# Performance work log

Hardware: AMD Instinct MI355X
Metric: run time of the kernel (lower is better)

The kernel has to match this reference:

```python
import math
import jax, jax.numpy as jnp
import numpy as np

B, N, D, H, L = 8, 128, 256, 8, 4
NOBJ, NREL = 150, 51
FF = 4 * D
Hd = D // H

def setup_inputs() -> dict:
    key = jax.random.key(0)
    ks = iter(jax.random.split(key, 80))
    def nrm(shape):
        return 0.02 * jax.random.normal(next(ks), shape, dtype=jnp.float32)
    inp = {}
    inp['obj_t'] = jax.random.randint(next(ks), (B, N), 0, NOBJ + 1)
    inp['rel_t'] = jax.random.randint(next(ks), (B, N, N), 0, NREL)
    inp['t'] = jax.random.randint(next(ks), (B,), 0, 1000)
    inp['node_mask'] = jnp.ones((B, N), dtype=bool)
    inp['edge_mask'] = jnp.ones((B, N, N), dtype=bool)
    # embeddings
    inp['obj_emb_table'] = nrm((NOBJ + 1, D))
    inp['rel_emb_table'] = nrm((NREL, D))
    # time mlp
    inp['time_w1'] = nrm((D, D)); inp['time_b1'] = jnp.zeros((D,), jnp.float32)
    inp['time_w2'] = nrm((D, D)); inp['time_b2'] = jnp.zeros((D,), jnp.float32)
    # per-layer stacked params [L, ...]
    inp['ln1_g'] = jnp.ones((L, D), jnp.float32); inp['ln1_b'] = jnp.zeros((L, D), jnp.float32)
    inp['q_w'] = nrm((L, D, D)); inp['q_b'] = jnp.zeros((L, D), jnp.float32)
    inp['k_w'] = nrm((L, D, D)); inp['k_b'] = jnp.zeros((L, D), jnp.float32)
    inp['v_w'] = nrm((L, D, D)); inp['v_b'] = jnp.zeros((L, D), jnp.float32)
    inp['o_w'] = nrm((L, D, D)); inp['o_b'] = jnp.zeros((L, D), jnp.float32)
    inp['eb_w'] = nrm((L, D, H)); inp['eb_b'] = jnp.zeros((L, H), jnp.float32)
    inp['ln2_g'] = jnp.ones((L, D), jnp.float32); inp['ln2_b'] = jnp.zeros((L, D), jnp.float32)
    inp['ff_w1'] = nrm((L, D, FF)); inp['ff_b1'] = jnp.zeros((L, FF), jnp.float32)
    inp['ff_w2'] = nrm((L, FF, D)); inp['ff_b2'] = jnp.zeros((L, D), jnp.float32)
    # heads
    inp['obj_head_w'] = nrm((D, NOBJ)); inp['obj_head_b'] = jnp.zeros((NOBJ,), jnp.float32)
    inp['subj_w'] = nrm((D, D)); inp['subj_b'] = jnp.zeros((D,), jnp.float32)
    inp['objp_w'] = nrm((D, D)); inp['objp_b'] = jnp.zeros((D,), jnp.float32)
    inp['eh_w1'] = nrm((4 * D, D)); inp['eh_b1'] = jnp.zeros((D,), jnp.float32)
    inp['eh_w2'] = nrm((D, 1)); inp['eh_b2'] = jnp.zeros((1,), jnp.float32)
    inp['rh_w1'] = nrm((4 * D, D)); inp['rh_b1'] = jnp.zeros((D,), jnp.float32)
    inp['rh_w2'] = nrm((D, NREL - 1)); inp['rh_b2'] = jnp.zeros((NREL - 1,), jnp.float32)
    return inp

def _ln(x, g, b, eps=1e-5):
    m = x.mean(-1, keepdims=True)
    v = ((x - m) ** 2).mean(-1, keepdims=True)
    return (x - m) / jnp.sqrt(v + eps) * g + b

def _timestep_emb(t, dim):
    half = dim // 2
    freqs = jnp.exp(-math.log(10000.0) * jnp.arange(half, dtype=jnp.float32) / half)
    args = t.astype(jnp.float32)[:, None] * freqs[None, :]
    return jnp.concatenate([jnp.cos(args), jnp.sin(args)], axis=-1)

def _gelu(x):
    return jax.nn.gelu(x, approximate=False)

def _forward(obj_t, rel_t, t, node_mask, edge_mask, p):
    nm = node_mask[..., None].astype(jnp.float32)  # [B,N,1]
    h = p['obj_emb_table'][obj_t]                  # [B,N,D]
    temb = _timestep_emb(t, D)
    temb = jax.nn.silu(temb @ p['time_w1'] + p['time_b1']) @ p['time_w2'] + p['time_b2']
    h = (h + temb[:, None, :]) * nm
    rel_emb = p['rel_emb_table'][rel_t]            # [B,N,N,D]
    scale = Hd ** -0.5
    for l in range(L):
        x = _ln(h, p['ln1_g'][l], p['ln1_b'][l])
        q = (x @ p['q_w'][l] + p['q_b'][l]).reshape(B, N, H, Hd)
        k = (x @ p['k_w'][l] + p['k_b'][l]).reshape(B, N, H, Hd)
        v = (x @ p['v_w'][l] + p['v_b'][l]).reshape(B, N, H, Hd)
        logits = jnp.einsum('bihd,bjhd->bhij', q, k) * scale
        bias = jnp.einsum('bijd,dh->bhij', rel_emb, p['eb_w'][l]) + p['eb_b'][l][None, :, None, None]
        logits = logits + bias
        logits = jnp.where(edge_mask[:, None, :, :], logits, -jnp.inf)
        logits = jnp.where(node_mask[:, None, None, :], logits, -jnp.inf)
        attn = jax.nn.softmax(logits, axis=-1)
        attn = jnp.nan_to_num(attn, nan=0.0, posinf=0.0, neginf=0.0)
        out = jnp.einsum('bhij,bjhd->bihd', attn, v).reshape(B, N, D)
        h = h + out @ p['o_w'][l] + p['o_b'][l]
        x2 = _ln(h, p['ln2_g'][l], p['ln2_b'][l])
        h = h + _gelu(x2 @ p['ff_w1'][l] + p['ff_b1'][l]) @ p['ff_w2'][l] + p['ff_b2'][l]
        h = h * nm
    obj_logits = h @ p['obj_head_w'] + p['obj_head_b']      # [B,N,NOBJ]
    subj_h = h @ p['subj_w'] + p['subj_b']
    obj_h = h @ p['objp_w'] + p['objp_b']
    hi = jnp.broadcast_to(subj_h[:, :, None, :], (B, N, N, D))
    hj = jnp.broadcast_to(obj_h[:, None, :, :], (B, N, N, D))
    pair_feat = jnp.concatenate([hi, hj, hi - hj, hi * hj], axis=-1)  # [B,N,N,4D]
    edge_logits = (_gelu(pair_feat @ p['eh_w1'] + p['eh_b1']) @ p['eh_w2'] + p['eh_b2'])[..., 0]
    rel_logits_pos = _gelu(pair_feat @ p['rh_w1'] + p['rh_b1']) @ p['rh_w2'] + p['rh_b2']
    return obj_logits, edge_logits, rel_logits_pos

PARAM_NAMES = ['obj_emb_table','rel_emb_table','time_w1','time_b1','time_w2','time_b2','ln1_g','ln1_b','q_w','q_b','k_w','k_b','v_w','v_b','o_w','o_b','eb_w','eb_b','ln2_g','ln2_b','ff_w1','ff_b1','ff_w2','ff_b2','obj_head_w','obj_head_b','subj_w','subj_b','objp_w','objp_b','eh_w1','eh_b1','eh_w2','eh_b2','rh_w1','rh_b1','rh_w2','rh_b2']

def reference(obj_t, rel_t, t, node_mask, edge_mask, obj_emb_table, rel_emb_table, time_w1, time_b1, time_w2, time_b2, ln1_g, ln1_b, q_w, q_b, k_w, k_b, v_w, v_b, o_w, o_b, eb_w, eb_b, ln2_g, ln2_b, ff_w1, ff_b1, ff_w2, ff_b2, obj_head_w, obj_head_b, subj_w, subj_b, objp_w, objp_b, eh_w1, eh_b1, eh_w2, eh_b2, rh_w1, rh_b1, rh_w2, rh_b2):
    loc = locals()
    p = {n: loc[n] for n in PARAM_NAMES}
    return _forward(obj_t, rel_t, t, node_mask, edge_mask, p)
```

## Files before the change

### kernel.cpp

```cpp
#include <hip/hip_runtime.h>
#include <hip/hip_bf16.h>
#include <math.h>

#define BB 8
#define NN 128
#define DD 256
#define HH 8
#define LL 4
#define FFD 1024
#define HD 32
#define NOBJ_ 150
#define NREL_ 51

typedef __attribute__((ext_vector_type(4))) float f32x4;
typedef __attribute__((ext_vector_type(8))) short s16x8;

__device__ __forceinline__ float erf_f(float x){
    float ax = fabsf(x);
    float t = __builtin_amdgcn_rcpf(1.f + 0.3275911f*ax);
    float y = t*(0.254829592f + t*(-0.284496736f + t*(1.421413741f +
              t*(-1.453152027f + t*1.061405429f))));
    float r = 1.f - y*__expf(-ax*ax);
    return copysignf(r, x);
}
__device__ __forceinline__ float gelu_f(float x){
    return 0.5f * x * (1.0f + erf_f(x * 0.70710678118654752f));
}
__device__ __forceinline__ ushort f2bf(float f){
    uint u = __float_as_uint(f);
    u += 0x7fff + ((u >> 16) & 1);
    return (ushort)(u >> 16);
}
__device__ __forceinline__ float bf2f(uint u){
    return __uint_as_float((u & 0xffffu) << 16);
}

__global__ __launch_bounds__(256) void k_init_h(const int* __restrict__ obj_t,
        const float* __restrict__ emb, const float* __restrict__ temb,
        float* __restrict__ h){
    int idx = blockIdx.x*256 + threadIdx.x;
    int d = idx & 255, n = (idx >> 8) & 127, b = idx >> 15;
    int o = obj_t[b*NN + n];
    h[idx] = emb[o*DD + d] + temb[b*DD + d];
}

__global__ __launch_bounds__(256) void k_lngemm(
        const float* __restrict__ A, const float* __restrict__ gw,
        const float* __restrict__ bw, const ushort* __restrict__ WT,
        const float* __restrict__ bias, ushort* __restrict__ Cb,
        int Nc, int act){
    __shared__ __align__(16) ushort As[8192];
    __shared__ __align__(16) ushort Ws[16384];
    int tid = threadIdx.x;
    int m0 = blockIdx.x*32, n0 = blockIdx.y*64;
    int r = tid >> 3, p = tid & 7;
    const float* ap = A + (size_t)(m0 + r)*256 + p*32;
    float x[32];
    float s1 = 0.f, s2 = 0.f;
    #pragma unroll
    for (int e4 = 0; e4 < 8; e4++){
        float4 v = *(const float4*)(ap + e4*4);
        x[e4*4+0]=v.x; x[e4*4+1]=v.y; x[e4*4+2]=v.z; x[e4*4+3]=v.w;
        s1 += v.x+v.y+v.z+v.w;
        s2 += v.x*v.x+v.y*v.y+v.z*v.z+v.w*v.w;
    }
    #pragma unroll
    for (int d = 1; d < 8; d <<= 1){
        s1 += __shfl_xor(s1, d, 64);
        s2 += __shfl_xor(s2, d, 64);
    }
    float mean = s1*(1.f/256.f);
    float var = s2*(1.f/256.f) - mean*mean;
    float rstd = rsqrtf(var + 1e-5f);
    #pragma unroll
    for (int j = 0; j < 4; j++){
        int kq = p*4 + j;
        uint o[4];
        #pragma unroll
        for (int pp = 0; pp < 4; pp++){
            int e = j*8 + pp*2;
            int k = p*32 + e;
            float v0 = (x[e]   - mean)*rstd*gw[k]   + bw[k];
            float v1 = (x[e+1] - mean)*rstd*gw[k+1] + bw[k+1];
            o[pp] = (uint)f2bf(v0) | ((uint)f2bf(v1) << 16);
        }
        int phys = r*32 + (kq ^ (r & 7));
        *(uint4*)(As + (size_t)phys*8) = make_uint4(o[0], o[1], o[2], o[3]);
    }
    #pragma unroll
    for (int rr = 0; rr < 8; rr++){
        int gi = tid + rr*256;
        int n = gi >> 5, kq = gi & 31;
        uint4 v = *(const uint4*)(WT + (size_t)(n0+n)*256 + kq*8);
        *(uint4*)(Ws + (size_t)(n*32 + (kq ^ (n&7)))*8) = v;
    }
    __syncthreads();
    int lane = tid & 63, w = tid >> 6, l15 = lane & 15, q = lane >> 4;
    f32x4 acc[2];
    acc[0] = (f32x4){0.f,0.f,0.f,0.f};
    acc[1] = (f32x4){0.f,0.f,0.f,0.f};
    int m = (w&1)*16 + l15;
    #pragma unroll
    for (int k0 = 0; k0 < 8; k0++){
        int kq = k0*4 + q;
        s16x8 af = *(const s16x8*)(As + (size_t)(m*32 + (kq ^ (m&7)))*8);
        #pragma unroll
        for (int t = 0; t < 2; t++){
            int n = ((w>>1)*2 + t)*16 + l15;
            s16x8 bf = *(const s16x8*)(Ws + (size_t)(n*32 + (kq ^ (n&7)))*8);
            acc[t] = __builtin_amdgcn_mfma_f32_16x16x32_bf16(af, bf, acc[t], 0, 0, 0);
        }
    }
    int mb = (w&1)*16;
    #pragma unroll
    for (int t = 0; t < 2; t++){
        int n = n0 + ((w>>1)*2 + t)*16 + l15;
        if (n < Nc){
// ... 252 lines not shown
        const float* __restrict__ objpw,
        const float* __restrict__ q_b, const float* __restrict__ k_b,
        const float* __restrict__ v_b,
        const float* __restrict__ subj_b, const float* __restrict__ objp_b,
        ushort* __restrict__ qkvT, ushort* __restrict__ oT,
        ushort* __restrict__ ff1T, ushort* __restrict__ ff2T,
        ushort* __restrict__ headT, ushort* __restrict__ sowT,
        float* __restrict__ qkvb, float* __restrict__ sob_b){
    int g = blockIdx.x*256 + threadIdx.x;
    if (g < 98304){
        int l = g / 24576, rem = g % 24576;
        int n = rem >> 5, kq = rem & 31;
        const float* src = (n < 256) ? q_w : (n < 512) ? k_w : v_w;
        int nn = n & 255;
        src += (size_t)l*65536;
        #pragma unroll
        for (int u = 0; u < 8; u++)
            qkvT[(size_t)g*8 + u] = f2bf(src[(size_t)(kq*8+u)*256 + nn]);
    } else if ((g -= 98304) < 32768){
        int l = g >> 13, rem = g & 8191;
        int n = rem >> 5, kq = rem & 31;
        const float* src = o_w + (size_t)l*65536;
        #pragma unroll
        for (int u = 0; u < 8; u++)
            oT[(size_t)g*8 + u] = f2bf(src[(size_t)(kq*8+u)*256 + n]);
    } else if ((g -= 32768) < 131072){
        int l = g >> 15, rem = g & 32767;
        int n = rem >> 5, kq = rem & 31;
        const float* src = ff1 + (size_t)l*262144;
        #pragma unroll
        for (int u = 0; u < 8; u++)
            ff1T[(size_t)g*8 + u] = f2bf(src[(size_t)(kq*8+u)*1024 + n]);
    } else if ((g -= 131072) < 131072){
        int l = g >> 15, rem = g & 32767;
        int n = rem >> 7, kq = rem & 127;
        const float* src = ff2 + (size_t)l*262144;
        #pragma unroll
        for (int u = 0; u < 8; u++)
            ff2T[(size_t)g*8 + u] = f2bf(src[(size_t)(kq*8+u)*256 + n]);
    } else if ((g -= 131072) < 6144){
        int n = g >> 5, kq = g & 31;
        #pragma unroll
        for (int u = 0; u < 8; u++)
            headT[(size_t)g*8 + u] = (n < NOBJ_) ? f2bf(headw[(size_t)(kq*8+u)*NOBJ_ + n]) : (ushort)0;
    } else if ((g -= 6144) < 16384){
        int n = g >> 5, kq = g & 31;
        const float* src = (n < 256) ? subjw : objpw;
        int nn = n & 255;
        #pragma unroll
        for (int u = 0; u < 8; u++)
            sowT[(size_t)g*8 + u] = f2bf(src[(size_t)(kq*8+u)*256 + nn]);
    } else if ((g -= 16384) < 384){
        #pragma unroll
        for (int u = 0; u < 8; u++){
            int flat = g*8 + u;
            int l = flat / 768, c = flat % 768;
            qkvb[flat] = (c < 256) ? q_b[l*256 + c] :
                         (c < 512) ? k_b[l*256 + c - 256] : v_b[l*256 + c - 512];
        }
    } else if ((g -= 384) < 64){
        #pragma unroll
        for (int u = 0; u < 8; u++){
            int c = g*8 + u;
            sob_b[c] = (c < 256) ? subj_b[c] : objp_b[c-256];
        }
    }
}

__global__ __launch_bounds__(256) void k_prep_obj(const float* __restrict__ sjhob,
        ushort* __restrict__ objf){
    int t = blockIdx.x*256 + threadIdx.x;
    int ai = t & 1023, kc = (t >> 10) & 3, b = t >> 12;
    int jt = ai >> 7, ks = (ai >> 6) & 1, lane = ai & 63;
    int j = jt*16 + (lane & 15);
    int k0 = kc*64 + ks*32 + (lane >> 4)*8;
    const float* src = sjhob + (size_t)(b*128 + j)*512 + 256 + k0;
    uint o[4];
    #pragma unroll
    for (int p = 0; p < 4; p++)
        o[p] = (uint)f2bf(src[p*2]) | ((uint)f2bf(src[p*2 + 1]) << 16);
    *(uint4*)(objf + (size_t)t*8) = make_uint4(o[0], o[1], o[2], o[3]);
}

__global__ __launch_bounds__(256, 3) void k_pair(
        const float* __restrict__ sjhob, const float* __restrict__ linI,
        const float* __restrict__ linJ, const ushort* __restrict__ objf,
        const ushort* __restrict__ w3fE, const ushort* __restrict__ w3fR,
        const ushort* __restrict__ w2fR, const float* __restrict__ eh_w2,
        const float* __restrict__ eh_b2, const float* __restrict__ rh_b2,
        float* __restrict__ edge_out, float* __restrict__ rel_out){
    __shared__ __align__(16) ushort U[8192];
    __shared__ __align__(16) float Rel[32*52];
    __shared__ __align__(16) float subj_sf[256];
    __shared__ __align__(16) float linEs[256];
    __shared__ __align__(16) float linRs[256];
    __shared__ __align__(16) float w2s[256];
    __shared__ __align__(16) float P[4][32];
    int tid = threadIdx.x;
    int bid = blockIdx.x;
    int jq = bid & 3, i = (bid >> 2) & 127, b = bid >> 9;
    int lane = tid & 63, w = tid >> 6;
    int l15 = lane & 15, q = lane >> 4;
    size_t rw = (size_t)(b*128 + i)*512;
    subj_sf[tid] = sjhob[rw + tid];
    linEs[tid]   = linI[rw + tid];
    linRs[tid]   = linI[rw + 256 + tid];
    w2s[tid]     = eh_w2[tid];
    __syncthreads();

    {
        int ks = (tid >> 6) & 1, qg = (tid >> 4) & 3;
        #pragma unroll
        for (int kc = 0; kc < 4; kc++){
            uint4 po = *(const uint4*)(objf + ((size_t)(b*4 + kc)*1024 + jq*256 + tid)*8);
            const float* sp = subj_sf + kc*64 + ks*32 + qg*8;
            uint oa[4] = {po.x, po.y, po.z, po.w};
            uint o[4];
            #pragma unroll
            for (int p = 0; p < 4; p++){
                float v0 = sp[p*2+0] * bf2f(oa[p]);
                float v1 = sp[p*2+1] * bf2f(oa[p] >> 16);
                o[p] = (uint)f2bf(v0) | ((uint)f2bf(v1) << 16);
            }
            *(uint4*)(U + (size_t)(kc*256 + tid)*8) = make_uint4(o[0], o[1], o[2], o[3]);
        }
    }
    __syncthreads();

    f32x4 aE[4][2];
    #pragma unroll
    for (int a = 0; a < 4; a++){
        aE[a][0] = (f32x4){0.f,0.f,0.f,0.f}; aE[a][1] = (f32x4){0.f,0.f,0.f,0.f};
    }
    #pragma unroll
    for (int kc = 0; kc < 4; kc++){
        const ushort* wbE = w3fE + (size_t)kc*16384;
        #pragma unroll
        for (int ks = 0; ks < 2; ks++){
            s16x8 bf0 = *(const s16x8*)(U + (size_t)(kc*256 + ks*64 + lane)*8);
            s16x8 bf1 = *(const s16x8*)(U + (size_t)(kc*256 + 128 + ks*64 + lane)*8);
            #pragma unroll
            for (int ct = 0; ct < 4; ct++){
                s16x8 af = *(const s16x8*)(wbE + (size_t)(((w*4+ct)*2 + ks)*64 + lane)*8);
                aE[ct][0] = __builtin_amdgcn_mfma_f32_16x16x32_bf16(af, bf0, aE[ct][0], 0, 0, 0);
                aE[ct][1] = __builtin_amdgcn_mfma_f32_16x16x32_bf16(af, bf1, aE[ct][1], 0, 0, 0);
            }
        }
    }
    {
        float part[2] = {0.f, 0.f};
        #pragma unroll
        for (int ct = 0; ct < 4; ct++){
            int cglob = (w*4 + ct)*16 + q*4;
            float li[4] = {linEs[cglob], linEs[cglob+1], linEs[cglob+2], linEs[cglob+3]};
            float ww[4] = {w2s[cglob], w2s[cglob+1], w2s[cglob+2], w2s[cglob+3]};
            #pragma unroll
            for (int jt = 0; jt < 2; jt++){
                int jg = jq*32 + jt*16 + l15;
                float4 lj = *(const float4*)(linJ + (size_t)(b*128 + jg)*512 + cglob);
                f32x4 v = aE[ct][jt];
                part[jt] += gelu_f(v.x + li[0] + lj.x) * ww[0];
                part[jt] += gelu_f(v.y + li[1] + lj.y) * ww[1];
                part[jt] += gelu_f(v.z + li[2] + lj.z) * ww[2];
                part[jt] += gelu_f(v.w + li[3] + lj.w) * ww[3];
            }
        }
        #pragma unroll
        for (int jt = 0; jt < 2; jt++){
            part[jt] += __shfl_xor(part[jt], 16, 64);
            part[jt] += __shfl_xor(part[jt], 32, 64);
            if (q == 0) P[w][jt*16 + l15] = part[jt];
        }
        __syncthreads();
        if (tid < 32){
            float s = eh_b2[0];
            #pragma unroll
            for (int u = 0; u < 4; u++) s += P[u][tid];
            edge_out[(size_t)(b*128 + i)*128 + jq*32 + tid] = s;
        }
    }

    f32x4 aR[4][2];
    #pragma unroll
    for (int a = 0; a < 4; a++){
        aR[a][0] = (f32x4){0.f,0.f,0.f,0.f}; aR[a][1] = (f32x4){0.f,0.f,0.f,0.f};
    }
    #pragma unroll
    for (int kc = 0; kc < 4; kc++){
        const ushort* wbR = w3fR + (size_t)kc*16384;
        #pragma unroll
        for (int ks = 0; ks < 2; ks++){
            s16x8 bf0 = *(const s16x8*)(U + (size_t)(kc*256 + ks*64 + lane)*8);
            s16x8 bf1 = *(const s16x8*)(U + (size_t)(kc*256 + 128 + ks*64 + lane)*8);
            #pragma unroll
            for (int ct = 0; ct < 4; ct++){
                s16x8 af = *(const s16x8*)(wbR + (size_t)(((w*4+ct)*2 + ks)*64 + lane)*8);
                aR[ct][0] = __builtin_amdgcn_mfma_f32_16x16x32_bf16(af, bf0, aR[ct][0], 0, 0, 0);
                aR[ct][1] = __builtin_amdgcn_mfma_f32_16x16x32_bf16(af, bf1, aR[ct][1], 0, 0, 0);
            }
        }
    }
    __syncthreads();

    #pragma unroll
    for (int ct = 0; ct < 4; ct++){
        int cglob = (w*4 + ct)*16 + q*4;
        float li0 = linRs[cglob],   li1 = linRs[cglob+1];
        float li2 = linRs[cglob+2], li3 = linRs[cglob+3];
        int cs = cglob >> 5, qg2 = (cglob >> 3) & 3, u0 = cglob & 7;
        #pragma unroll
        for (int jt = 0; jt < 2; jt++){
            int jg = jq*32 + jt*16 + l15;
            float4 lj = *(const float4*)(linJ + (size_t)(b*128 + jg)*512 + 256 + cglob);
            f32x4 v = aR[ct][jt];
            ushort g0 = f2bf(gelu_f(v.x + li0 + lj.x));
            ushort g1 = f2bf(gelu_f(v.y + li1 + lj.y));
            ushort g2 = f2bf(gelu_f(v.z + li2 + lj.z));
            ushort g3 = f2bf(gelu_f(v.w + li3 + lj.w));
            uint2 pk = make_uint2((uint)g0 | ((uint)g1 << 16),
                                  (uint)g2 | ((uint)g3 << 16));
            uint off = (uint)(((jt*8 + cs)*64 + qg2*16 + l15)*16 + u0*2);
            *(uint2*)((char*)U + off) = pk;
        }
    }
    __syncthreads();
    f32x4 acc2[2];
    acc2[0] = (f32x4){0.f,0.f,0.f,0.f};
    acc2[1] = (f32x4){0.f,0.f,0.f,0.f};
    #pragma unroll
    for (int cs = 0; cs < 8; cs++){
        s16x8 a2 = *(const s16x8*)(w2fR + (size_t)((cs*4 + w)*64 + lane)*8);
        #pragma unroll
        for (int jt = 0; jt < 2; jt++){
            s16x8 b2 = *(const s16x8*)(U + (size_t)((jt*8 + cs)*64 + lane)*8);
            acc2[jt] = __builtin_amdgcn_mfma_f32_16x16x32_bf16(a2, b2, acc2[jt], 0, 0, 0);
        }
    }
    #pragma unroll
    for (int jt = 0; jt < 2; jt++){
        int jl = jt*16 + l15;
        float vv[4] = {acc2[jt].x, acc2[jt].y, acc2[jt].z, acc2[jt].w};
        #pragma unroll
        for (int rg = 0; rg < 4; rg++){
            int r = w*16 + q*4 + rg;
            if (r < 50) Rel[jl*52 + r] = vv[rg] + rh_b2[r];
        }
    }
    __syncthreads();
    size_t obase = ((size_t)(b*128 + i)*128 + jq*32)*50;
    for (int s = tid; s < 1600; s += 256){
        int j = s / 50, r = s - j*50;
        rel_out[obase + s] = Rel[j*52 + r];
    }
}

extern "C" void kernel_launch(void* const* d_in, const int* in_sizes, int n_in,
                              void* d_out, int out_size, void* d_ws, size_t ws_size,
                              hipStream_t stream){
    const int*   obj_t     = (const int*)d_in[0];
    const int*   rel_t     = (const int*)d_in[1];
    const int*   t_in      = (const int*)d_in[2];
    const float* obj_emb   = (const float*)d_in[5];
    const float* rel_emb   = (const float*)d_in[6];
    const float* time_w1   = (const float*)d_in[7];
    const float* time_b1   = (const float*)d_in[8];
    const float* time_w2   = (const float*)d_in[9];
    const float* time_b2   = (const float*)d_in[10];
    const float* ln1_g     = (const float*)d_in[11];
    const float* ln1_b     = (const float*)d_in[12];
    const float* q_w       = (const float*)d_in[13];
    const float* q_b       = (const float*)d_in[14];
    const float* k_w       = (const float*)d_in[15];
    const float* k_b       = (const float*)d_in[16];
    const float* v_w       = (const float*)d_in[17];
    const float* v_b       = (const float*)d_in[18];
    const float* o_w       = (const float*)d_in[19];
    const float* o_b       = (const float*)d_in[20];
    const float* eb_w      = (const float*)d_in[21];
    const float* eb_b      = (const float*)d_in[22];
    const float* ln2_g     = (const float*)d_in[23];
    const float* ln2_b     = (const float*)d_in[24];
    const float* ff_w1     = (const float*)d_in[25];
    const float* ff_b1     = (const float*)d_in[26];
    const float* ff_w2     = (const float*)d_in[27];
    const float* ff_b2     = (const float*)d_in[28];
    const float* obj_hw    = (const float*)d_in[29];
    const float* obj_hb    = (const float*)d_in[30];
    const float* subj_w    = (const float*)d_in[31];
    const float* subj_b    = (const float*)d_in[32];
    const float* objp_w    = (const float*)d_in[33];
    const float* objp_b    = (const float*)d_in[34];
    const float* eh_w1     = (const float*)d_in[35];
    const float* eh_b1     = (const float*)d_in[36];
    const float* eh_w2     = (const float*)d_in[37];
    const float* eh_b2     = (const float*)d_in[38];
    const float* rh_w1     = (const float*)d_in[39];
    const float* rh_b1     = (const float*)d_in[40];
    const float* rh_w2     = (const float*)d_in[41];
    const float* rh_b2     = (const float*)d_in[42];

    float* out = (float*)d_out;
    float* obj_logits  = out;
    float* edge_logits = out + 153600;
    float* rel_logits  = out + 284672;

    float* w = (float*)d_ws;
    float* temb    = w;  w += 2048;
    float* hbuf    = w;  w += 262144;
    float* relb    = w;  w += 2048;
    float* linI    = w;  w += 524288;
    float* linJ    = w;  w += 524288;
    float* biascat = w;  w += 1024;
    float* qkvb    = w;  w += 4096;
    float* sob_b   = w;  w += 512;
    float* sjhob   = w;  w += 524288;
    ushort* us     = (ushort*)w;
    ushort* qkv16  = us;  us += 786432;
    ushort* aob16  = us;  us += 262144;
    ushort* ff1b16 = us;  us += 1048576;
    ushort* hb16   = us;  us += 262144;
    ushort* sjhob16= us;  us += 524288;
    ushort* w3fE   = us;  us += 65536;
    ushort* w3fR   = us;  us += 65536;
    ushort* w2fR   = us;  us += 16384;
    ushort* wicatT = us;  us += 131072;
    ushort* wjT    = us;  us += 131072;
    ushort* objf   = us;  us += 262144;
    ushort* qkvT   = us;  us += 786432;
    ushort* oT     = us;  us += 262144;
    ushort* ff1T   = us;  us += 1048576;
    ushort* ff2T   = us;  us += 1048576;
    ushort* headT  = us;  us += 49152;
    ushort* sowT   = us;  us += 131072;

    k_prep_w<<<215, 256, 0, stream>>>(eh_w1, rh_w1, rh_w2, eh_b1, rh_b1,
                                      rel_emb, eb_w, eb_b,
                                      t_in, time_w1, time_b1, time_w2, time_b2,
                                      w3fE, w3fR, wjT, w2fR, wicatT, biascat,
                                      relb, temb);
    k_prep_bw<<<1626, 256, 0, stream>>>(q_w, k_w, v_w, o_w, ff_w1, ff_w2,
                                        obj_hw, subj_w, objp_w, q_b, k_b, v_b,
                                        subj_b, objp_b,
                                        qkvT, oT, ff1T, ff2T, headT, sowT, qkvb, sob_b);
    k_init_h<<<1024, 256, 0, stream>>>(obj_t, obj_emb, temb, hbuf);

    for (int l = 0; l < LL; l++){
        k_lngemm<<<dim3(32,12), 256, 0, stream>>>(hbuf, ln1_g + l*DD, ln1_b + l*DD,
                qkvT + (size_t)l*196608, qkvb + l*768, qkv16, 768, 0);
        k_attn<<<256, 256, 0, stream>>>(qkv16, rel_t, relb + l*NREL_*HH, aob16);
        k_bgemm<<<dim3(32,4), 256, 0, stream>>>(aob16, oT + (size_t)l*65536,
                o_b + l*DD, hbuf, hbuf, nullptr, 256, 256, 256, 256, 256, 0, 0, 0, 0, 0);
        k_lngemm<<<dim3(32,16), 256, 0, stream>>>(hbuf, ln2_g + l*DD, ln2_b + l*DD,
                ff1T + (size_t)l*262144, ff_b1 + l*FFD, ff1b16, 1024, 1);
        k_bgemm<<<dim3(32,4), 256, 0, stream>>>(ff1b16, ff2T + (size_t)l*262144,
                ff_b2 + l*DD, hbuf, hbuf, hb16, 1024, 256, 1024, 1024, 256, 0, 0, 0, 0, 0);
    }

    k_bgemm<<<dim3(32,3), 256, 0, stream>>>(hb16, headT, obj_hb,
            nullptr, obj_logits, nullptr, 256, 150, 256, 256, 150, 0, 0, 0, 0, 0);
    k_bgemm<<<dim3(32,8), 256, 0, stream>>>(hb16, sowT, sob_b,
            nullptr, sjhob, sjhob16, 256, 512, 256, 256, 512, 0, 0, 0, 0, 0);
    k_prep_obj<<<128, 256, 0, stream>>>(sjhob, objf);
    k_bgemm<<<dim3(32,8,2), 256, 0, stream>>>(sjhob16, wicatT, biascat,
            nullptr, linI, nullptr, 256, 512, 512, 256, 512, 0,
            256, 131072, 524288, 512);

    k_pair<<<4096, 256, 0, stream>>>(sjhob, linI, linJ, objf, w3fE, w3fR,
                                     w2fR, eh_w2, eh_b2, rh_b2,
                                     edge_logits, rel_logits);
}
```

Before: 506.0 us.

## Process two i-rows per k_pair block and fuse edge/rel first-layer GEMMs

k_pair now runs 512-thread blocks that each cover two query rows i, halving the grid. Each weight fragment loaded from global memory is reused across both rows, and the edge and relation first-layer MFMA loops are merged into one pass over the shared U tile. The objf loads are issued before the first barrier, and the Rel staging buffer is aliased onto U to limit LDS growth. In exchange, register pressure rises (aE and aR live at once), LDS per block grows, and occupancy may drop to two blocks of 512 threads.

```diff
diff --git a/kernel.cpp b/kernel.cpp
--- a/kernel.cpp
+++ b/kernel.cpp
@@ -451,39 +451,45 @@
     *(uint4*)(objf + (size_t)t*8) = make_uint4(o[0], o[1], o[2], o[3]);
 }
 
-__global__ __launch_bounds__(256, 3) void k_pair(
+__global__ __launch_bounds__(512, 2) void k_pair(
         const float* __restrict__ sjhob, const float* __restrict__ linI,
         const float* __restrict__ linJ, const ushort* __restrict__ objf,
         const ushort* __restrict__ w3fE, const ushort* __restrict__ w3fR,
         const ushort* __restrict__ w2fR, const float* __restrict__ eh_w2,
         const float* __restrict__ eh_b2, const float* __restrict__ rh_b2,
         float* __restrict__ edge_out, float* __restrict__ rel_out){
-    __shared__ __align__(16) ushort U[8192];
-    __shared__ __align__(16) float Rel[32*52];
-    __shared__ __align__(16) float subj_sf[256];
-    __shared__ __align__(16) float linEs[256];
-    __shared__ __align__(16) float linRs[256];
+    __shared__ __align__(16) ushort U[16384];
+    __shared__ __align__(16) float subj_sf[512];
+    __shared__ __align__(16) float linEs[512];
+    __shared__ __align__(16) float linRs[512];
     __shared__ __align__(16) float w2s[256];
-    __shared__ __align__(16) float P[4][32];
+    __shared__ __align__(16) float P[8][2][32];
     int tid = threadIdx.x;
     int bid = blockIdx.x;
-    int jq = bid & 3, i = (bid >> 2) & 127, b = bid >> 9;
+    int jq = bid & 3, i2 = (bid >> 2) & 63, b = bid >> 8;
+    int i0 = i2*2;
     int lane = tid & 63, w = tid >> 6;
     int l15 = lane & 15, q = lane >> 4;
-    size_t rw = (size_t)(b*128 + i)*512;
-    subj_sf[tid] = sjhob[rw + tid];
-    linEs[tid]   = linI[rw + tid];
-    linRs[tid]   = linI[rw + 256 + tid];
-    w2s[tid]     = eh_w2[tid];
-    __syncthreads();
-
+    int r = tid & 255, il = tid >> 8;
     {
-        int ks = (tid >> 6) & 1, qg = (tid >> 4) & 3;
+        size_t rw = (size_t)(b*128 + i0 + il)*512;
+        subj_sf[tid] = sjhob[rw + r];
+        linEs[tid]   = linI[rw + r];
+        linRs[tid]   = linI[rw + 256 + r];
+        if (tid < 256) w2s[tid] = eh_w2[tid];
+    }
+    uint4 po[4];
+    #pragma unroll
+    for (int kc = 0; kc < 4; kc++)
+        po[kc] = *(const uint4*)(objf + (((size_t)(b*4 + kc)*1024) + jq*256 + r)*8);
+    __syncthreads();
+
+    {
+        int ks2 = (r >> 6) & 1, qg = (r >> 4) & 3;
         #pragma unroll
         for (int kc = 0; kc < 4; kc++){
-            uint4 po = *(const uint4*)(objf + ((size_t)(b*4 + kc)*1024 + jq*256 + tid)*8);
-            const float* sp = subj_sf + kc*64 + ks*32 + qg*8;
-            uint oa[4] = {po.x, po.y, po.z, po.w};
+            const float* sp = subj_sf + il*256 + kc*64 + ks2*32 + qg*8;
+            uint oa[4] = {po[kc].x, po[kc].y, po[kc].z, po[kc].w};
             uint o[4];
             #pragma unroll
             for (int p = 0; p < 4; p++){
@@ -491,135 +497,148 @@
                 float v1 = sp[p*2+1] * bf2f(oa[p] >> 16);
                 o[p] = (uint)f2bf(v0) | ((uint)f2bf(v1) << 16);
             }
-            *(uint4*)(U + (size_t)(kc*256 + tid)*8) = make_uint4(o[0], o[1], o[2], o[3]);
-        }
-    }
-    __syncthreads();
-
-    f32x4 aE[4][2];
-    #pragma unroll
-    for (int a = 0; a < 4; a++){
-        aE[a][0] = (f32x4){0.f,0.f,0.f,0.f}; aE[a][1] = (f32x4){0.f,0.f,0.f,0.f};
-    }
+            *(uint4*)(U + (size_t)(kc*512 + il*256 + r)*8) = make_uint4(o[0],o[1],o[2],o[3]);
+        }
+    }
+    __syncthreads();
+
+    f32x4 aE[2][2][2], aR[2][2][2];
+    #pragma unroll
+    for (int c2 = 0; c2 < 2; c2++)
+        #pragma unroll
+        for (int i = 0; i < 2; i++)
+            #pragma unroll
+            for (int jt = 0; jt < 2; jt++){
+                aE[c2][i][jt] = (f32x4){0.f,0.f,0.f,0.f};
+                aR[c2][i][jt] = (f32x4){0.f,0.f,0.f,0.f};
+            }
     #pragma unroll
     for (int kc = 0; kc < 4; kc++){
         const ushort* wbE = w3fE + (size_t)kc*16384;
+        const ushort* wbR = w3fR + (size_t)kc*16384;
         #pragma unroll
         for (int ks = 0; ks < 2; ks++){
-            s16x8 bf0 = *(const s16x8*)(U + (size_t)(kc*256 + ks*64 + lane)*8);
-            s16x8 bf1 = *(const s16x8*)(U + (size_t)(kc*256 + 128 + ks*64 + lane)*8);
-            #pragma unroll
-            for (int ct = 0; ct < 4; ct++){
-                s16x8 af = *(const s16x8*)(wbE + (size_t)(((w*4+ct)*2 + ks)*64 + lane)*8);
-                aE[ct][0] = __builtin_amdgcn_mfma_f32_16x16x32_bf16(af, bf0, aE[ct][0], 0, 0, 0);
-                aE[ct][1] = __builtin_amdgcn_mfma_f32_16x16x32_bf16(af, bf1, aE[ct][1], 0, 0, 0);
-            }
-        }
-    }
+            s16x8 bf[2][2];
+            #pragma unroll
+            for (int i = 0; i < 2; i++)
+                #pragma unroll
+                for (int jt = 0; jt < 2; jt++)
+                    bf[i][jt] = *(const s16x8*)(U + (size_t)(kc*512 + i*256 + jt*128 + ks*64 + lane)*8);
+            #pragma unroll
+            for (int c2 = 0; c2 < 2; c2++){
+                int ct = w*2 + c2;
+                s16x8 afE = *(const s16x8*)(wbE + (size_t)((ct*2 + ks)*64 + lane)*8);
+                #pragma unroll
+                for (int i = 0; i < 2; i++){
+                    aE[c2][i][0] = __builtin_amdgcn_mfma_f32_16x16x32_bf16(afE, bf[i][0], aE[c2][i][0], 0, 0, 0);
+                    aE[c2][i][1] = __builtin_amdgcn_mfma_f32_16x16x32_bf16(afE, bf[i][1], aE[c2][i][1], 0, 0, 0);
+                }
+                s16x8 afR = *(const s16x8*)(wbR + (size_t)((ct*2 + ks)*64 + lane)*8);
+                #pragma unroll
+                for (int i = 0; i < 2; i++){
+                    aR[c2][i][0] = __builtin_amdgcn_mfma_f32_16x16x32_bf16(afR, bf[i][0], aR[c2][i][0], 0, 0, 0);
+                    aR[c2][i][1] = __builtin_amdgcn_mfma_f32_16x16x32_bf16(afR, bf[i][1], aR[c2][i][1], 0, 0, 0);
+                }
+            }
+        }
+    }
+
     {
-        float part[2] = {0.f, 0.f};
-        #pragma unroll
-        for (int ct = 0; ct < 4; ct++){
-            int cglob = (w*4 + ct)*16 + q*4;
-            float li[4] = {linEs[cglob], linEs[cglob+1], linEs[cglob+2], linEs[cglob+3]};
-            float ww[4] = {w2s[cglob], w2s[cglob+1], w2s[cglob+2], w2s[cglob+3]};
+        float part[2][2] = {{0.f,0.f},{0.f,0.f}};
+        #pragma unroll
+        for (int c2 = 0; c2 < 2; c2++){
+            int cglob = (w*2 + c2)*16 + q*4;
+            float ww0 = w2s[cglob], ww1 = w2s[cglob+1];
+            float ww2 = w2s[cglob+2], ww3 = w2s[cglob+3];
             #pragma unroll
             for (int jt = 0; jt < 2; jt++){
                 int jg = jq*32 + jt*16 + l15;
                 float4 lj = *(const float4*)(linJ + (size_t)(b*128 + jg)*512 + cglob);
-                f32x4 v = aE[ct][jt];
-                part[jt] += gelu_f(v.x + li[0] + lj.x) * ww[0];
-                part[jt] += gelu_f(v.y + li[1] + lj.y) * ww[1];
-                part[jt] += gelu_f(v.z + li[2] + lj.z) * ww[2];
-                part[jt] += gelu_f(v.w + li[3] + lj.w) * ww[3];
-            }
-        }
-        #pragma unroll
-        for (int jt = 0; jt < 2; jt++){
-            part[jt] += __shfl_xor(part[jt], 16, 64);
-            part[jt] += __shfl_xor(part[jt], 32, 64);
-            if (q == 0) P[w][jt*16 + l15] = part[jt];
-        }
+                #pragma unroll
+                for (int i = 0; i < 2; i++){
+                    const float* li = linEs + i*256 + cglob;
+                    f32x4 v = aE[c2][i][jt];
+                    part[i][jt] += gelu_f(v.x + li[0] + lj.x) * ww0;
+                    part[i][jt] += gelu_f(v.y + li[1] + lj.y) * ww1;
+                    part[i][jt] += gelu_f(v.z + li[2] + lj.z) * ww2;
+                    part[i][jt] += gelu_f(v.w + li[3] + lj.w) * ww3;
+                }
+            }
+        }
+        #pragma unroll
+        for (int i = 0; i < 2; i++)
+            #pragma unroll
+            for (int jt = 0; jt < 2; jt++){
+                float pv = part[i][jt];
+                pv += __shfl_xor(pv, 16, 64);
+                pv += __shfl_xor(pv, 32, 64);
+                if (q == 0) P[w][i][jt*16 + l15] = pv;
+            }
         __syncthreads();
-        if (tid < 32){
+        if (tid < 64){
+            int i = tid >> 5, jl = tid & 31;
             float s = eh_b2[0];
             #pragma unroll
-            for (int u = 0; u < 4; u++) s += P[u][tid];
-            edge_out[(size_t)(b*128 + i)*128 + jq*32 + tid] = s;
-        }
-    }
-
-    f32x4 aR[4][2];
-    #pragma unroll
-    for (int a = 0; a < 4; a++){
-        aR[a][0] = (f32x4){0.f,0.f,0.f,0.f}; aR[a][1] = (f32x4){0.f,0.f,0.f,0.f};
-    }
-    #pragma unroll
-    for (int kc = 0; kc < 4; kc++){
-        const ushort* wbR = w3fR + (size_t)kc*16384;
-        #pragma unroll
-        for (int ks = 0; ks < 2; ks++){
-            s16x8 bf0 = *(const s16x8*)(U + (size_t)(kc*256 + ks*64 + lane)*8);
-            s16x8 bf1 = *(const s16x8*)(U + (size_t)(kc*256 + 128 + ks*64 + lane)*8);
-            #pragma unroll
-            for (int ct = 0; ct < 4; ct++){
-                s16x8 af = *(const s16x8*)(wbR + (size_t)(((w*4+ct)*2 + ks)*64 + lane)*8);
-                aR[ct][0] = __builtin_amdgcn_mfma_f32_16x16x32_bf16(af, bf0, aR[ct][0], 0, 0, 0);
-                aR[ct][1] = __builtin_amdgcn_mfma_f32_16x16x32_bf16(af, bf1, aR[ct][1], 0, 0, 0);
-            }
-        }
-    }
-    __syncthreads();
-
-    #pragma unroll
-    for (int ct = 0; ct < 4; ct++){
-        int cglob = (w*4 + ct)*16 + q*4;
-        float li0 = linRs[cglob],   li1 = linRs[cglob+1];
-        float li2 = linRs[cglob+2], li3 = linRs[cglob+3];
+            for (int u = 0; u < 8; u++) s += P[u][i][jl];
+            edge_out[(size_t)(b*128 + i0 + i)*128 + jq*32 + jl] = s;
+        }
+    }
+
+    #pragma unroll
+    for (int c2 = 0; c2 < 2; c2++){
+        int cglob = (w*2 + c2)*16 + q*4;
         int cs = cglob >> 5, qg2 = (cglob >> 3) & 3, u0 = cglob & 7;
         #pragma unroll
         for (int jt = 0; jt < 2; jt++){
             int jg = jq*32 + jt*16 + l15;
             float4 lj = *(const float4*)(linJ + (size_t)(b*128 + jg)*512 + 256 + cglob);
-            f32x4 v = aR[ct][jt];
-            ushort g0 = f2bf(gelu_f(v.x + li0 + lj.x));
-            ushort g1 = f2bf(gelu_f(v.y + li1 + lj.y));
-            ushort g2 = f2bf(gelu_f(v.z + li2 + lj.z));
-            ushort g3 = f2bf(gelu_f(v.w + li3 + lj.w));
-            uint2 pk = make_uint2((uint)g0 | ((uint)g1 << 16),
-                                  (uint)g2 | ((uint)g3 << 16));
-            uint off = (uint)(((jt*8 + cs)*64 + qg2*16 + l15)*16 + u0*2);
-            *(uint2*)((char*)U + off) = pk;
+            #pragma unroll
+            for (int i = 0; i < 2; i++){
+                const float* li = linRs + i*256 + cglob;
+                f32x4 v = aR[c2][i][jt];
+                ushort g0 = f2bf(gelu_f(v.x + li[0] + lj.x));
+                ushort g1 = f2bf(gelu_f(v.y + li[1] + lj.y));
+                ushort g2 = f2bf(gelu_f(v.z + li[2] + lj.z));
+                ushort g3 = f2bf(gelu_f(v.w + li[3] + lj.w));
+                uint2 pk = make_uint2((uint)g0 | ((uint)g1 << 16),
+                                      (uint)g2 | ((uint)g3 << 16));
+                uint off = (uint)(i*16384 + (((jt*8 + cs)*64 + qg2*16 + l15)*16 + u0*2));
+                *(uint2*)((char*)U + off) = pk;
+            }
         }
     }
     __syncthreads();
     f32x4 acc2[2];
     acc2[0] = (f32x4){0.f,0.f,0.f,0.f};
     acc2[1] = (f32x4){0.f,0.f,0.f,0.f};
+    int isel = w >> 2, rt = w & 3;
     #pragma unroll
     for (int cs = 0; cs < 8; cs++){
-        s16x8 a2 = *(const s16x8*)(w2fR + (size_t)((cs*4 + w)*64 + lane)*8);
+        s16x8 a2 = *(const s16x8*)(w2fR + (size_t)((cs*4 + rt)*64 + lane)*8);
         #pragma unroll
         for (int jt = 0; jt < 2; jt++){
-            s16x8 b2 = *(const s16x8*)(U + (size_t)((jt*8 + cs)*64 + lane)*8);
+            s16x8 b2 = *(const s16x8*)(U + (size_t)(isel*1024 + (jt*8 + cs)*64 + lane)*8);
             acc2[jt] = __builtin_amdgcn_mfma_f32_16x16x32_bf16(a2, b2, acc2[jt], 0, 0, 0);
         }
     }
+    __syncthreads();
+    float* Rel = (float*)U;
     #pragma unroll
     for (int jt = 0; jt < 2; jt++){
         int jl = jt*16 + l15;
         float vv[4] = {acc2[jt].x, acc2[jt].y, acc2[jt].z, acc2[jt].w};
         #pragma unroll
         for (int rg = 0; rg < 4; rg++){
-            int r = w*16 + q*4 + rg;
-            if (r < 50) Rel[jl*52 + r] = vv[rg] + rh_b2[r];
-        }
-    }
-    __syncthreads();
-    size_t obase = ((size_t)(b*128 + i)*128 + jq*32)*50;
-    for (int s = tid; s < 1600; s += 256){
-        int j = s / 50, r = s - j*50;
-        rel_out[obase + s] = Rel[j*52 + r];
+            int rr = rt*16 + q*4 + rg;
+            if (rr < 50) Rel[(isel*32 + jl)*52 + rr] = vv[rg] + rh_b2[rr];
+        }
+    }
+    __syncthreads();
+    size_t obase = ((size_t)(b*128 + i0)*128 + jq*32)*50;
+    for (int s = tid; s < 3200; s += 512){
+        int iw = s / 1600, rem = s - iw*1600;
+        int j = rem / 50, rr = rem - j*50;
+        rel_out[obase + (size_t)iw*6400 + j*50 + rr] = Rel[(iw*32 + j)*52 + rr];
     }
 }
 
@@ -734,7 +753,7 @@
             nullptr, linI, nullptr, 256, 512, 512, 256, 512, 0,
             256, 131072, 524288, 512);
 
-    k_pair<<<4096, 256, 0, stream>>>(sjhob, linI, linJ, objf, w3fE, w3fR,
+    k_pair<<<2048, 512, 0, stream>>>(sjhob, linI, linJ, objf, w3fE, w3fR,
                                      w2fR, eh_w2, eh_b2, rh_b2,
                                      edge_logits, rel_logits);
 }
```

After: 518.0 us. +2.4%, slower.

## Split pair kernel into separate edge-head and relation-head blocks

Applied to the files above, without the earlier changes.

Each k_pair block now handles only one of the two pair-head branches (edge or relation), chosen by a new low bit of the block index, and the grid doubles to 8192 blocks. This halves per-block MFMA work and register/LDS state, raises the launch-bound occupancy hint from 3 to 4 waves, and prefetches the objf loads before the first barrier. The cost is that the shared prologue (subj*obj product staging into LDS, loading objf) is now done twice per (b,i,jq), and edge blocks finish early, which can unbalance work across blocks.

```diff
diff --git a/kernel.cpp b/kernel.cpp
--- a/kernel.cpp
+++ b/kernel.cpp
@@ -451,7 +451,7 @@
     *(uint4*)(objf + (size_t)t*8) = make_uint4(o[0], o[1], o[2], o[3]);
 }
 
-__global__ __launch_bounds__(256, 3) void k_pair(
+__global__ __launch_bounds__(256, 4) void k_pair(
         const float* __restrict__ sjhob, const float* __restrict__ linI,
         const float* __restrict__ linJ, const ushort* __restrict__ objf,
         const ushort* __restrict__ w3fE, const ushort* __restrict__ w3fR,
@@ -461,29 +461,31 @@
     __shared__ __align__(16) ushort U[8192];
     __shared__ __align__(16) float Rel[32*52];
     __shared__ __align__(16) float subj_sf[256];
-    __shared__ __align__(16) float linEs[256];
-    __shared__ __align__(16) float linRs[256];
+    __shared__ __align__(16) float linS[256];
     __shared__ __align__(16) float w2s[256];
     __shared__ __align__(16) float P[4][32];
     int tid = threadIdx.x;
     int bid = blockIdx.x;
-    int jq = bid & 3, i = (bid >> 2) & 127, b = bid >> 9;
+    int h2 = bid & 1;
+    int jq = (bid >> 1) & 3, i = (bid >> 3) & 127, b = bid >> 10;
     int lane = tid & 63, w = tid >> 6;
     int l15 = lane & 15, q = lane >> 4;
     size_t rw = (size_t)(b*128 + i)*512;
     subj_sf[tid] = sjhob[rw + tid];
-    linEs[tid]   = linI[rw + tid];
-    linRs[tid]   = linI[rw + 256 + tid];
-    w2s[tid]     = eh_w2[tid];
+    linS[tid]    = linI[rw + (h2 ? 256 : 0) + tid];
+    if (!h2) w2s[tid] = eh_w2[tid];
+    uint4 po[4];
+    #pragma unroll
+    for (int kc = 0; kc < 4; kc++)
+        po[kc] = *(const uint4*)(objf + (((size_t)(b*4 + kc)*1024) + jq*256 + tid)*8);
     __syncthreads();
 
     {
-        int ks = (tid >> 6) & 1, qg = (tid >> 4) & 3;
+        int ks2 = (tid >> 6) & 1, qg = (tid >> 4) & 3;
         #pragma unroll
         for (int kc = 0; kc < 4; kc++){
-            uint4 po = *(const uint4*)(objf + ((size_t)(b*4 + kc)*1024 + jq*256 + tid)*8);
-            const float* sp = subj_sf + kc*64 + ks*32 + qg*8;
-            uint oa[4] = {po.x, po.y, po.z, po.w};
+            const float* sp = subj_sf + kc*64 + ks2*32 + qg*8;
+            uint oa[4] = {po[kc].x, po[kc].y, po[kc].z, po[kc].w};
             uint o[4];
             #pragma unroll
             for (int p = 0; p < 4; p++){
@@ -491,43 +493,46 @@
                 float v1 = sp[p*2+1] * bf2f(oa[p] >> 16);
                 o[p] = (uint)f2bf(v0) | ((uint)f2bf(v1) << 16);
             }
-            *(uint4*)(U + (size_t)(kc*256 + tid)*8) = make_uint4(o[0], o[1], o[2], o[3]);
-        }
-    }
-    __syncthreads();
-
-    f32x4 aE[4][2];
+            *(uint4*)(U + (size_t)(kc*256 + tid)*8) = make_uint4(o[0],o[1],o[2],o[3]);
+        }
+    }
+    __syncthreads();
+
+    const ushort* w3 = h2 ? w3fR : w3fE;
+    f32x4 acc[4][2];
     #pragma unroll
     for (int a = 0; a < 4; a++){
-        aE[a][0] = (f32x4){0.f,0.f,0.f,0.f}; aE[a][1] = (f32x4){0.f,0.f,0.f,0.f};
+        acc[a][0] = (f32x4){0.f,0.f,0.f,0.f};
+        acc[a][1] = (f32x4){0.f,0.f,0.f,0.f};
     }
     #pragma unroll
     for (int kc = 0; kc < 4; kc++){
-        const ushort* wbE = w3fE + (size_t)kc*16384;
+        const ushort* wb = w3 + (size_t)kc*16384;
         #pragma unroll
         for (int ks = 0; ks < 2; ks++){
             s16x8 bf0 = *(const s16x8*)(U + (size_t)(kc*256 + ks*64 + lane)*8);
             s16x8 bf1 = *(const s16x8*)(U + (size_t)(kc*256 + 128 + ks*64 + lane)*8);
             #pragma unroll
             for (int ct = 0; ct < 4; ct++){
-                s16x8 af = *(const s16x8*)(wbE + (size_t)(((w*4+ct)*2 + ks)*64 + lane)*8);
-                aE[ct][0] = __builtin_amdgcn_mfma_f32_16x16x32_bf16(af, bf0, aE[ct][0], 0, 0, 0);
-                aE[ct][1] = __builtin_amdgcn_mfma_f32_16x16x32_bf16(af, bf1, aE[ct][1], 0, 0, 0);
+                s16x8 af = *(const s16x8*)(wb + (size_t)(((w*4+ct)*2 + ks)*64 + lane)*8);
+                acc[ct][0] = __builtin_amdgcn_mfma_f32_16x16x32_bf16(af, bf0, acc[ct][0], 0, 0, 0);
+                acc[ct][1] = __builtin_amdgcn_mfma_f32_16x16x32_bf16(af, bf1, acc[ct][1], 0, 0, 0);
             }
         }
     }
-    {
+
+    if (!h2){
         float part[2] = {0.f, 0.f};
         #pragma unroll
         for (int ct = 0; ct < 4; ct++){
             int cglob = (w*4 + ct)*16 + q*4;
-            float li[4] = {linEs[cglob], linEs[cglob+1], linEs[cglob+2], linEs[cglob+3]};
+            float li[4] = {linS[cglob], linS[cglob+1], linS[cglob+2], linS[cglob+3]};
             float ww[4] = {w2s[cglob], w2s[cglob+1], w2s[cglob+2], w2s[cglob+3]};
             #pragma unroll
             for (int jt = 0; jt < 2; jt++){
                 int jg = jq*32 + jt*16 + l15;
                 float4 lj = *(const float4*)(linJ + (size_t)(b*128 + jg)*512 + cglob);
-                f32x4 v = aE[ct][jt];
+                f32x4 v = acc[ct][jt];
                 part[jt] += gelu_f(v.x + li[0] + lj.x) * ww[0];
                 part[jt] += gelu_f(v.y + li[1] + lj.y) * ww[1];
                 part[jt] += gelu_f(v.z + li[2] + lj.z) * ww[2];
@@ -547,41 +552,21 @@
             for (int u = 0; u < 4; u++) s += P[u][tid];
             edge_out[(size_t)(b*128 + i)*128 + jq*32 + tid] = s;
         }
-    }
-
-    f32x4 aR[4][2];
-    #pragma unroll
-    for (int a = 0; a < 4; a++){
-        aR[a][0] = (f32x4){0.f,0.f,0.f,0.f}; aR[a][1] = (f32x4){0.f,0.f,0.f,0.f};
-    }
-    #pragma unroll
-    for (int kc = 0; kc < 4; kc++){
-        const ushort* wbR = w3fR + (size_t)kc*16384;
-        #pragma unroll
-        for (int ks = 0; ks < 2; ks++){
-            s16x8 bf0 = *(const s16x8*)(U + (size_t)(kc*256 + ks*64 + lane)*8);
-            s16x8 bf1 = *(const s16x8*)(U + (size_t)(kc*256 + 128 + ks*64 + lane)*8);
-            #pragma unroll
-            for (int ct = 0; ct < 4; ct++){
-                s16x8 af = *(const s16x8*)(wbR + (size_t)(((w*4+ct)*2 + ks)*64 + lane)*8);
-                aR[ct][0] = __builtin_amdgcn_mfma_f32_16x16x32_bf16(af, bf0, aR[ct][0], 0, 0, 0);
-                aR[ct][1] = __builtin_amdgcn_mfma_f32_16x16x32_bf16(af, bf1, aR[ct][1], 0, 0, 0);
-            }
-        }
-    }
-    __syncthreads();
-
+        return;
+    }
+
+    __syncthreads();
     #pragma unroll
     for (int ct = 0; ct < 4; ct++){
         int cglob = (w*4 + ct)*16 + q*4;
-        float li0 = linRs[cglob],   li1 = linRs[cglob+1];
-        float li2 = linRs[cglob+2], li3 = linRs[cglob+3];
+        float li0 = linS[cglob],   li1 = linS[cglob+1];
+        float li2 = linS[cglob+2], li3 = linS[cglob+3];
         int cs = cglob >> 5, qg2 = (cglob >> 3) & 3, u0 = cglob & 7;
         #pragma unroll
         for (int jt = 0; jt < 2; jt++){
             int jg = jq*32 + jt*16 + l15;
             float4 lj = *(const float4*)(linJ + (size_t)(b*128 + jg)*512 + 256 + cglob);
-            f32x4 v = aR[ct][jt];
+            f32x4 v = acc[ct][jt];
             ushort g0 = f2bf(gelu_f(v.x + li0 + lj.x));
             ushort g1 = f2bf(gelu_f(v.y + li1 + lj.y));
             ushort g2 = f2bf(gelu_f(v.z + li2 + lj.z));
@@ -734,7 +719,7 @@
             nullptr, linI, nullptr, 256, 512, 512, 256, 512, 0,
             256, 131072, 524288, 512);
 
-    k_pair<<<4096, 256, 0, stream>>>(sjhob, linI, linJ, objf, w3fE, w3fR,
+    k_pair<<<8192, 256, 0, stream>>>(sjhob, linI, linJ, objf, w3fE, w3fR,
                                      w2fR, eh_w2, eh_b2, rh_b2,
                                      edge_logits, rel_logits);
 }
```

After: 509.7 us. No clear change (+0.7%).

## Merge edge and relation first-layer MFMA loops and use packed bf16 conversion

Applied to the files above, without the earlier changes.

In the pair-head kernel, the edge-head and relation-head first-layer MFMA loops are merged into one pass. Each B fragment read from LDS is reused for both weight sets, and the weight fragments are preloaded ahead of the MFMAs. The objf and linJ global loads are issued earlier so their latency overlaps other work, which removes a barrier between the two GEMM phases. Manual bf16 rounding is replaced with the hardware v_cvt_pk_bf16_f32 instruction. In exchange, register pressure roughly doubles (16 accumulator vectors plus preloaded fragments), which may lower occupancy or cause spills.

```diff
diff --git a/kernel.cpp b/kernel.cpp
--- a/kernel.cpp
+++ b/kernel.cpp
@@ -33,6 +33,11 @@
 }
 __device__ __forceinline__ float bf2f(uint u){
     return __uint_as_float((u & 0xffffu) << 16);
+}
+__device__ __forceinline__ uint cvtpk_bf16(float lo, float hi){
+    uint r;
+    asm("v_cvt_pk_bf16_f32 %0, %1, %2" : "=v"(r) : "v"(lo), "v"(hi));
+    return r;
 }
 
 __global__ __launch_bounds__(256) void k_init_h(const int* __restrict__ obj_t,
@@ -475,48 +480,74 @@
     linEs[tid]   = linI[rw + tid];
     linRs[tid]   = linI[rw + 256 + tid];
     w2s[tid]     = eh_w2[tid];
+    uint4 po[4];
+    #pragma unroll
+    for (int kc = 0; kc < 4; kc++)
+        po[kc] = *(const uint4*)(objf + (((size_t)(b*4 + kc)*1024) + jq*256 + tid)*8);
     __syncthreads();
 
     {
-        int ks = (tid >> 6) & 1, qg = (tid >> 4) & 3;
+        int ks2 = (tid >> 6) & 1, qg = (tid >> 4) & 3;
         #pragma unroll
         for (int kc = 0; kc < 4; kc++){
-            uint4 po = *(const uint4*)(objf + ((size_t)(b*4 + kc)*1024 + jq*256 + tid)*8);
-            const float* sp = subj_sf + kc*64 + ks*32 + qg*8;
-            uint oa[4] = {po.x, po.y, po.z, po.w};
+            const float* sp = subj_sf + kc*64 + ks2*32 + qg*8;
+            uint oa[4] = {po[kc].x, po[kc].y, po[kc].z, po[kc].w};
             uint o[4];
             #pragma unroll
             for (int p = 0; p < 4; p++){
                 float v0 = sp[p*2+0] * bf2f(oa[p]);
                 float v1 = sp[p*2+1] * bf2f(oa[p] >> 16);
-                o[p] = (uint)f2bf(v0) | ((uint)f2bf(v1) << 16);
-            }
-            *(uint4*)(U + (size_t)(kc*256 + tid)*8) = make_uint4(o[0], o[1], o[2], o[3]);
-        }
-    }
-    __syncthreads();
-
-    f32x4 aE[4][2];
+                o[p] = cvtpk_bf16(v0, v1);
+            }
+            *(uint4*)(U + (size_t)(kc*256 + tid)*8) = make_uint4(o[0],o[1],o[2],o[3]);
+        }
+    }
+    __syncthreads();
+
+    f32x4 aE[4][2], aR[4][2];
     #pragma unroll
     for (int a = 0; a < 4; a++){
         aE[a][0] = (f32x4){0.f,0.f,0.f,0.f}; aE[a][1] = (f32x4){0.f,0.f,0.f,0.f};
+        aR[a][0] = (f32x4){0.f,0.f,0.f,0.f}; aR[a][1] = (f32x4){0.f,0.f,0.f,0.f};
     }
     #pragma unroll
     for (int kc = 0; kc < 4; kc++){
         const ushort* wbE = w3fE + (size_t)kc*16384;
+        const ushort* wbR = w3fR + (size_t)kc*16384;
         #pragma unroll
         for (int ks = 0; ks < 2; ks++){
             s16x8 bf0 = *(const s16x8*)(U + (size_t)(kc*256 + ks*64 + lane)*8);
             s16x8 bf1 = *(const s16x8*)(U + (size_t)(kc*256 + 128 + ks*64 + lane)*8);
+            s16x8 afE_[4], afR_[4];
             #pragma unroll
             for (int ct = 0; ct < 4; ct++){
-                s16x8 af = *(const s16x8*)(wbE + (size_t)(((w*4+ct)*2 + ks)*64 + lane)*8);
-                aE[ct][0] = __builtin_amdgcn_mfma_f32_16x16x32_bf16(af, bf0, aE[ct][0], 0, 0, 0);
-                aE[ct][1] = __builtin_amdgcn_mfma_f32_16x16x32_bf16(af, bf1, aE[ct][1], 0, 0, 0);
-            }
-        }
-    }
+                afE_[ct] = *(const s16x8*)(wbE + (size_t)(((w*4+ct)*2 + ks)*64 + lane)*8);
+                afR_[ct] = *(const s16x8*)(wbR + (size_t)(((w*4+ct)*2 + ks)*64 + lane)*8);
+            }
+            #pragma unroll
+            for (int ct = 0; ct < 4; ct++){
+                aE[ct][0] = __builtin_amdgcn_mfma_f32_16x16x32_bf16(afE_[ct], bf0, aE[ct][0], 0, 0, 0);
+                aE[ct][1] = __builtin_amdgcn_mfma_f32_16x16x32_bf16(afE_[ct], bf1, aE[ct][1], 0, 0, 0);
+            }
+            #pragma unroll
+            for (int ct = 0; ct < 4; ct++){
+                aR[ct][0] = __builtin_amdgcn_mfma_f32_16x16x32_bf16(afR_[ct], bf0, aR[ct][0], 0, 0, 0);
+                aR[ct][1] = __builtin_amdgcn_mfma_f32_16x16x32_bf16(afR_[ct], bf1, aR[ct][1], 0, 0, 0);
+            }
+        }
+    }
+
     {
+        float4 ljE[8];
+        #pragma unroll
+        for (int ct = 0; ct < 4; ct++){
+            int cglob = (w*4 + ct)*16 + q*4;
+            #pragma unroll
+            for (int jt = 0; jt < 2; jt++){
+                int jg = jq*32 + jt*16 + l15;
+                ljE[ct*2+jt] = *(const float4*)(linJ + (size_t)(b*128 + jg)*512 + cglob);
+            }
+        }
         float part[2] = {0.f, 0.f};
         #pragma unroll
         for (int ct = 0; ct < 4; ct++){
@@ -525,8 +556,7 @@
             float ww[4] = {w2s[cglob], w2s[cglob+1], w2s[cglob+2], w2s[cglob+3]};
             #pragma unroll
             for (int jt = 0; jt < 2; jt++){
-                int jg = jq*32 + jt*16 + l15;
-                float4 lj = *(const float4*)(linJ + (size_t)(b*128 + jg)*512 + cglob);
+                float4 lj = ljE[ct*2+jt];
                 f32x4 v = aE[ct][jt];
                 part[jt] += gelu_f(v.x + li[0] + lj.x) * ww[0];
                 part[jt] += gelu_f(v.y + li[1] + lj.y) * ww[1];
@@ -549,47 +579,35 @@
         }
     }
 
-    f32x4 aR[4][2];
-    #pragma unroll
-    for (int a = 0; a < 4; a++){
-        aR[a][0] = (f32x4){0.f,0.f,0.f,0.f}; aR[a][1] = (f32x4){0.f,0.f,0.f,0.f};
-    }
-    #pragma unroll
-    for (int kc = 0; kc < 4; kc++){
-        const ushort* wbR = w3fR + (size_t)kc*16384;
-        #pragma unroll
-        for (int ks = 0; ks < 2; ks++){
-            s16x8 bf0 = *(const s16x8*)(U + (size_t)(kc*256 + ks*64 + lane)*8);
-            s16x8 bf1 = *(const s16x8*)(U + (size_t)(kc*256 + 128 + ks*64 + lane)*8);
-            #pragma unroll
-            for (int ct = 0; ct < 4; ct++){
-                s16x8 af = *(const s16x8*)(wbR + (size_t)(((w*4+ct)*2 + ks)*64 + lane)*8);
-                aR[ct][0] = __builtin_amdgcn_mfma_f32_16x16x32_bf16(af, bf0, aR[ct][0], 0, 0, 0);
-                aR[ct][1] = __builtin_amdgcn_mfma_f32_16x16x32_bf16(af, bf1, aR[ct][1], 0, 0, 0);
-            }
-        }
-    }
-    __syncthreads();
-
-    #pragma unroll
-    for (int ct = 0; ct < 4; ct++){
-        int cglob = (w*4 + ct)*16 + q*4;
-        float li0 = linRs[cglob],   li1 = linRs[cglob+1];
-        float li2 = linRs[cglob+2], li3 = linRs[cglob+3];
-        int cs = cglob >> 5, qg2 = (cglob >> 3) & 3, u0 = cglob & 7;
-        #pragma unroll
-        for (int jt = 0; jt < 2; jt++){
-            int jg = jq*32 + jt*16 + l15;
-            float4 lj = *(const float4*)(linJ + (size_t)(b*128 + jg)*512 + 256 + cglob);
-            f32x4 v = aR[ct][jt];
-            ushort g0 = f2bf(gelu_f(v.x + li0 + lj.x));
-            ushort g1 = f2bf(gelu_f(v.y + li1 + lj.y));
-            ushort g2 = f2bf(gelu_f(v.z + li2 + lj.z));
-            ushort g3 = f2bf(gelu_f(v.w + li3 + lj.w));
-            uint2 pk = make_uint2((uint)g0 | ((uint)g1 << 16),
-                                  (uint)g2 | ((uint)g3 << 16));
-            uint off = (uint)(((jt*8 + cs)*64 + qg2*16 + l15)*16 + u0*2);
-            *(uint2*)((char*)U + off) = pk;
+    {
+        float4 ljR[8];
+        #pragma unroll
+        for (int ct = 0; ct < 4; ct++){
+            int cglob = (w*4 + ct)*16 + q*4;
+            #pragma unroll
+            for (int jt = 0; jt < 2; jt++){
+                int jg = jq*32 + jt*16 + l15;
+                ljR[ct*2+jt] = *(const float4*)(linJ + (size_t)(b*128 + jg)*512 + 256 + cglob);
+            }
+        }
+        #pragma unroll
+        for (int ct = 0; ct < 4; ct++){
+            int cglob = (w*4 + ct)*16 + q*4;
+            float li0 = linRs[cglob],   li1 = linRs[cglob+1];
+            float li2 = linRs[cglob+2], li3 = linRs[cglob+3];
+            int cs = cglob >> 5, qg2 = (cglob >> 3) & 3, u0 = cglob & 7;
+            #pragma unroll
+            for (int jt = 0; jt < 2; jt++){
+                float4 lj = ljR[ct*2+jt];
+                f32x4 v = aR[ct][jt];
+                float g0 = gelu_f(v.x + li0 + lj.x);
+                float g1 = gelu_f(v.y + li1 + lj.y);
+                float g2 = gelu_f(v.z + li2 + lj.z);
+                float g3 = gelu_f(v.w + li3 + lj.w);
+                uint2 pk = make_uint2(cvtpk_bf16(g0, g1), cvtpk_bf16(g2, g3));
+                uint off = (uint)(((jt*8 + cs)*64 + qg2*16 + l15)*16 + u0*2);
+                *(uint2*)((char*)U + off) = pk;
+            }
         }
     }
     __syncthreads();
```

Result: slower. 526.9 us (+4.1%).
